# Performance work log

Measured on AMD Instinct MI355X. Metric: run time of the kernel, lower is better.

## Reference

```python
import jax, jax.numpy as jnp
import numpy as np

B, T, F = 32, 512, 4096
H = 128            # num_lstm
NUM_CLASSES = 2    # dense outputs = NUM_CLASSES + 1 (CTC blank)


def setup_inputs() -> dict:
    key = jax.random.key(0)
    ks = jax.random.split(key, 6)
    x = jax.random.normal(ks[0], (B, T, F), dtype=jnp.float32)
    # Keras LSTM params: kernel [F, 4H], recurrent_kernel [H, 4H], bias [4H]
    # (gate order i, f, c, o). Glorot-ish scaling for stability.
    Wk = jax.random.normal(ks[1], (F, 4 * H), dtype=jnp.float32) / np.sqrt(F)
    Wr = jax.random.normal(ks[2], (H, 4 * H), dtype=jnp.float32) / np.sqrt(H)
    b = jnp.zeros((4 * H,), dtype=jnp.float32).at[H:2 * H].set(1.0)  # unit_forget_bias
    Wd = jax.random.normal(ks[3], (H, NUM_CLASSES + 1), dtype=jnp.float32) / np.sqrt(H)
    bd = jnp.zeros((NUM_CLASSES + 1,), dtype=jnp.float32)
    return {"x": x, "Wk": Wk, "Wr": Wr, "b": b, "Wd": Wd, "bd": bd}


def _lstm(x, Wk, Wr, b):
    # Precompute input projections for all timesteps (big GEMM once).
    z = jnp.einsum("btf,fg->btg", x, Wk) + b          # [B, T, 4H]
    z = jnp.transpose(z, (1, 0, 2))                    # [T, B, 4H]

    def step(carry, z_t):
        h, c = carry
        g = z_t + h @ Wr                               # [B, 4H]
        i = jax.nn.sigmoid(g[:, 0 * H:1 * H])
        f = jax.nn.sigmoid(g[:, 1 * H:2 * H])
        cc = jnp.tanh(g[:, 2 * H:3 * H])
        o = jax.nn.sigmoid(g[:, 3 * H:4 * H])
        c = f * c + i * cc
        h = o * jnp.tanh(c)
        return (h, c), h

    h0 = jnp.zeros((x.shape[0], H), dtype=x.dtype)
    c0 = jnp.zeros((x.shape[0], H), dtype=x.dtype)
    _, hs = jax.lax.scan(step, (h0, c0), z)            # hs: [T, B, H]
    return jnp.transpose(hs, (1, 0, 2))                # [B, T, H]


def reference(x, Wk, Wr, b, Wd, bd):
    # Inference-mode forward (dropout/recurrent_dropout inactive).
    h = _lstm(x, Wk, Wr, b)                            # [B, T, H]
    return h @ Wd + bd                                 # [B, T, num_classes+1]
```

## Files before the change

### kernel.cpp

```cpp
#include <hip/hip_runtime.h>
#include <hip/hip_bf16.h>
#include <hip/hip_fp16.h>
#include <math.h>

#define B_  32
#define T_  512
#define F_  4096
#define H_  128
#define G4H 512
#define NCLS 3
#define M_  (B_ * T_)
#define KSTEPS 128

typedef _Float16 f16x8 __attribute__((ext_vector_type(8)));
typedef _Float16 f16x4 __attribute__((ext_vector_type(4)));
typedef float    f32x4 __attribute__((ext_vector_type(4)));

__global__ __launch_bounds__(256) void cvt_wkT(
    const float* __restrict__ Wk, _Float16* __restrict__ btK)
{
    __shared__ float ls[64][65];
    const int k0 = blockIdx.x * 64;
    const int n0 = blockIdx.y * 64;
    const int tid = threadIdx.x;

    {
        int r  = tid >> 4;
        int c4 = (tid & 15) * 4;
        #pragma unroll
        for (int p = 0; p < 4; ++p) {
            float4 v = *reinterpret_cast<const float4*>(
                &Wk[(size_t)(k0 + r + p * 16) * G4H + n0 + c4]);
            ls[r + p * 16][c4 + 0] = v.x;
            ls[r + p * 16][c4 + 1] = v.y;
            ls[r + p * 16][c4 + 2] = v.z;
            ls[r + p * 16][c4 + 3] = v.w;
        }
    }
    __syncthreads();
    {
        int rn = tid >> 2;
        int ck = (tid & 3) * 16;
        f16x8 h0, h1;
        #pragma unroll
        for (int j = 0; j < 8; ++j) {
            h0[j] = (_Float16)ls[ck + j][rn];
            h1[j] = (_Float16)ls[ck + 8 + j][rn];
        }
        const int n    = n0 + rn;
        const int kg   = k0 + ck;
        const int kblk = kg >> 5;
        const int kk   = kg & 31;
        const int g0   = kk >> 3;
        const int sw   = (n >> 1) & 3;
        _Float16* base = btK + (size_t)kblk * (512 * 32) + (size_t)n * 32;
        *reinterpret_cast<f16x8*>(base + ((g0 ^ sw) << 3))       = h0;
        *reinterpret_cast<f16x8*>(base + (((g0 + 1) ^ sw) << 3)) = h1;
    }
}

__global__ __launch_bounds__(256) void cvt_wrT(
    const float* __restrict__ Wr, _Float16* __restrict__ wrT)
{
    __shared__ float ls[64][65];
    const int k0 = blockIdx.x * 64;
    const int n0 = blockIdx.y * 64;
    const int tid = threadIdx.x;
    {
        int r  = tid >> 4;
        int c4 = (tid & 15) * 4;
        #pragma unroll
        for (int p = 0; p < 4; ++p) {
            float4 v = *reinterpret_cast<const float4*>(
                &Wr[(size_t)(k0 + r + p * 16) * G4H + n0 + c4]);
            ls[r + p * 16][c4 + 0] = v.x;
            ls[r + p * 16][c4 + 1] = v.y;
            ls[r + p * 16][c4 + 2] = v.z;
            ls[r + p * 16][c4 + 3] = v.w;
        }
    }
    __syncthreads();
    {
        int rn = tid >> 2;
        int ck = (tid & 3) * 16;
        f16x8 h0, h1;
        #pragma unroll
        for (int j = 0; j < 8; ++j) {
            h0[j] = (_Float16)ls[ck + j][rn];
            h1[j] = (_Float16)ls[ck + 8 + j][rn];
        }
        _Float16* dst = &wrT[(size_t)(n0 + rn) * H_ + k0 + ck];
        *reinterpret_cast<f16x8*>(dst)     = h0;
        *reinterpret_cast<f16x8*>(dst + 8) = h1;
    }
}

__device__ __forceinline__ void lds_barrier() {
    asm volatile("s_waitcnt lgkmcnt(0)" ::: "memory");
    __builtin_amdgcn_s_barrier();
    asm volatile("" ::: "memory");
}

__global__ __launch_bounds__(256, 4) void gemm_fused(
    const float* __restrict__ x, const _Float16* __restrict__ btK,
    const float* __restrict__ bias, float* __restrict__ z)
{
    __shared__ __align__(16) _Float16 As[2][64 * 32];

    const int tid = threadIdx.x;
    const int w   = tid >> 6;
    const int l   = tid & 63;
    const int fr  = l & 15;
    const int q   = l >> 4;

    const int bid   = blockIdx.x;
    const int xcd   = bid & 7;
    const int idx   = bid >> 3;
    const int mt    = xcd * 32 + (idx >> 2);
    const int ntile = idx & 3;
    const int m0    = mt * 64;
    const int n0    = ntile * 128;

    const int ar = tid >> 3;
    const int hc = (tid & 7) * 4;
    const int abyte = ((((hc >> 3) ^ ((ar >> 1) & 3)) << 4) | ((hc << 1) & 15));
    const float* xrow0 = x + (size_t)(m0 + ar) * F_ + hc;
    const float* xrow1 = xrow0 + (size_t)32 * F_;

    const int nA = n0 + w * 32 + fr;
    const int nB = nA + 16;
    const _Float16* bp0 = btK + (size_t)nA * 32 + ((q ^ ((nA >> 1) & 3)) << 3);
    const _Float16* bp1 = btK + (size_t)nB * 32 + ((q ^ ((nB >> 1) & 3)) << 3);

    #define LOADB(t, bfv)                                                     \
    {                                                                         \
        bfv[0] = *reinterpret_cast<const f16x8*>(bp0 + (size_t)(t) * 16384);  \
        bfv[1] = *reinterpret_cast<const f16x8*>(bp1 + (size_t)(t) * 16384);  \
    }

    #define LOADX(t, va, vb)                                                  \
    {                                                                         \
        va = *reinterpret_cast<const float4*>(xrow0 + (size_t)(t) * 32);      \
        vb = *reinterpret_cast<const float4*>(xrow1 + (size_t)(t) * 32);      \
    }

    #define WRITE_A(va, vb, buf)                                              \
    {                                                                         \
        f16x4 h0; h0[0] = (_Float16)va.x; h0[1] = (_Float16)va.y;             \
        h0[2] = (_Float16)va.z; h0[3] = (_Float16)va.w;                       \
        f16x4 h1; h1[0] = (_Float16)vb.x; h1[1] = (_Float16)vb.y;             \
        h1[2] = (_Float16)vb.z; h1[3] = (_Float16)vb.w;                       \
        char* ab = reinterpret_cast<char*>(&As[buf][0]);                      \
        *reinterpret_cast<f16x4*>(ab + ar * 64 + abyte) = h0;                 \
        *reinterpret_cast<f16x4*>(ab + (ar + 32) * 64 + abyte) = h1;          \
    }

    #define COMPUTE(buf, bfv)                                                 \
    {                                                                         \
        f16x8 af[4];                                                          \
        _Pragma("unroll")                                                     \
        for (int i = 0; i < 4; ++i) {                                         \
            int r   = i * 16 + fr;                                            \
            int off = r * 64 + ((q ^ ((r >> 1) & 3)) << 4);                   \
            af[i] = *reinterpret_cast<const f16x8*>(                          \
                reinterpret_cast<const char*>(&As[buf][0]) + off);            \
        }                                                                     \
        _Pragma("unroll")                                                     \
        for (int i = 0; i < 4; ++i)                                           \
            _Pragma("unroll")                                                 \
            for (int j = 0; j < 2; ++j)                                       \
                acc[i][j] = __builtin_amdgcn_mfma_f32_16x16x32_f16(           \
                    af[i], bfv[j], acc[i][j], 0, 0, 0);                       \
    }

    f32x4 acc[4][2] = {};
    f16x8 bfA[2], bfB[2];
    float4 xa0, xa1, xb0, xb1;

    LOADX(0, xa0, xa1) LOADX(1, xb0, xb1)
    LOADB(0, bfA) LOADB(1, bfB)
    WRITE_A(xa0, xa1, 0)
    lds_barrier();

    for (int t = 0; t < 126; t += 2) {
        LOADX(t + 2, xa0, xa1)
        WRITE_A(xb0, xb1, 1)
        COMPUTE(0, bfA)
        LOADB(t + 2, bfA)
        lds_barrier();
        LOADX(t + 3, xb0, xb1)
        WRITE_A(xa0, xa1, 0)
        COMPUTE(1, bfB)
        LOADB(t + 3, bfB)
        lds_barrier();
    }
    WRITE_A(xb0, xb1, 1)
    COMPUTE(0, bfA)
    lds_barrier();
    COMPUTE(1, bfB)

    #undef LOADB
    #undef LOADX
    #undef WRITE_A
    #undef COMPUTE

    #pragma unroll
    for (int j = 0; j < 2; ++j) {
        const int nn = n0 + w * 32 + j * 16 + fr;
        const float bj = bias[nn];
        #pragma unroll
        for (int i = 0; i < 4; ++i)
            #pragma unroll
            for (int r = 0; r < 4; ++r)
                z[(size_t)(m0 + i * 16 + q * 4 + r) * G4H + nn]
                    = acc[i][j][r] + bj;
    }
}

__device__ __forceinline__ float sig_f(float x) {
    return __builtin_amdgcn_rcpf(
        1.0f + __builtin_amdgcn_exp2f(-1.442695040888963f * x));
}
__device__ __forceinline__ float tanh_f(float x) {
    return 1.0f - 2.0f * __builtin_amdgcn_rcpf(
        1.0f + __builtin_amdgcn_exp2f(2.885390081777927f * x));
}

__global__ __launch_bounds__(512, 2) void lstm_mfma(
    const float* __restrict__ z,
    const _Float16* __restrict__ wrT,
    float* __restrict__ hs,
    float* __restrict__ cst,
    _Float16* __restrict__ h16,
    int t0)
{
    const int b    = blockIdx.x;
    const int tid  = threadIdx.x;
    const int w    = tid >> 6;
    const int lane = tid & 63;
    const int l15  = lane & 15;
    const int q    = lane >> 4;
    const int jj   = w * 16 + l15;

    __shared__ __align__(16) _Float16 hA[2][128];

    f16x8 bf[4][4];
    #pragma unroll
    for (int g = 0; g < 4; ++g)
        #pragma unroll
        for (int kf = 0; kf < 4; ++kf)
            bf[g][kf] = *reinterpret_cast<const f16x8*>(
                &wrT[(size_t)(g * H_ + jj) * H_ + kf * 32 + q * 8]);

    float cstate;
    if (t0 == 0) {
        if (tid < 128) reinterpret_cast<unsigned int*>(hA)[tid] = 0u;
        cstate = 0.f;
    } else {
        if (tid < 64)
            reinterpret_cast<unsigned int*>(hA[0])[tid] =
                reinterpret_cast<const unsigned int*>(h16 + (size_t)b * H_)[tid];
        cstate = cst[(size_t)b * H_ + jj];
    }

    const float* zq    = z  + (size_t)b * T_ * G4H + jj;
    float*       hbase = hs + (size_t)b * T_ * H_;

    const f32x4 zero4 = {0.f, 0.f, 0.f, 0.f};

    #define LOADZ(t, d)                                                       \
    {                                                                         \
        int zo = (((t) & (T_ - 1)) << 9);                                     \
        d.x = zq[zo];       d.y = zq[zo + 128];                               \
        d.z = zq[zo + 256]; d.w = zq[zo + 384];                               \
    }

    float4 zP0, zP1, zP2, zP3;
    LOADZ(t0 + 0, zP0) LOADZ(t0 + 1, zP1)
    LOADZ(t0 + 2, zP2) LOADZ(t0 + 3, zP3)

    __syncthreads();

    #define LSTM_STEP(t, CUR, ZZ)                                             \
    {                                                                         \
        f16x8 af0 = *reinterpret_cast<const f16x8*>(&hA[CUR][0 * 32 + q * 8]);\
        f16x8 af1 = *reinterpret_cast<const f16x8*>(&hA[CUR][1 * 32 + q * 8]);\
        f16x8 af2 = *reinterpret_cast<const f16x8*>(&hA[CUR][2 * 32 + q * 8]);\
        f16x8 af3 = *reinterpret_cast<const f16x8*>(&hA[CUR][3 * 32 + q * 8]);\
        float zt0_ = ZZ.x, zt1_ = ZZ.y, zt2_ = ZZ.z, zt3_ = ZZ.w;             \
        LOADZ((t) + 4, ZZ)                                                    \
        float gv[4];                                                          \
        _Pragma("unroll")                                                     \
        for (int g = 0; g < 4; ++g) {                                         \
            f32x4 aA = __builtin_amdgcn_mfma_f32_16x16x32_f16(                \
                af0, bf[g][0], zero4, 0, 0, 0);                               \
            aA = __builtin_amdgcn_mfma_f32_16x16x32_f16(                      \
                af1, bf[g][1], aA, 0, 0, 0);                                  \
            f32x4 aB = __builtin_amdgcn_mfma_f32_16x16x32_f16(                \
                af2, bf[g][2], zero4, 0, 0, 0);                               \
            aB = __builtin_amdgcn_mfma_f32_16x16x32_f16(                      \
                af3, bf[g][3], aB, 0, 0, 0);                                  \
            gv[g] = aA[0] + aB[0];                                            \
        }                                                                     \
        float iv = sig_f(gv[0] + zt0_);                                       \
        float fv = sig_f(gv[1] + zt1_);                                       \
        float cc = tanh_f(gv[2] + zt2_);                                      \
        float ov = sig_f(gv[3] + zt3_);                                       \
        cstate = fv * cstate + iv * cc;                                       \
        float h = ov * tanh_f(cstate);                                        \
        if (q == 0) {                                                         \
            hA[CUR ^ 1][jj] = (_Float16)h;                                    \
            hbase[((t) << 7) + jj] = h;                                       \
        }                                                                     \
        lds_barrier();                                                        \
    }

    for (int t = t0; t < t0 + 256; t += 4) {
        LSTM_STEP(t,     0, zP0)
        LSTM_STEP(t + 1, 1, zP1)
        LSTM_STEP(t + 2, 0, zP2)
        LSTM_STEP(t + 3, 1, zP3)
    }
    #undef LSTM_STEP
    #undef LOADZ

    if (q == 0) cst[(size_t)b * H_ + jj] = cstate;
    if (tid < 64)
        reinterpret_cast<unsigned int*>(h16 + (size_t)b * H_)[tid] =
            reinterpret_cast<unsigned int*>(hA[0])[tid];
}

__global__ __launch_bounds__(256) void dense_out(
    const float* __restrict__ hs, const float* __restrict__ Wd,
    const float* __restrict__ bd, float* __restrict__ out)
{
    int idx = blockIdx.x * 256 + threadIdx.x;
    if (idx >= B_ * T_ * NCLS) return;
    int cls = idx % NCLS;
    int row = idx / NCLS;
    const float* h = hs + (size_t)row * H_;
    float acc = bd[cls];
    #pragma unroll 8
    for (int k = 0; k < H_; ++k) acc += h[k] * Wd[k * NCLS + cls];
    out[idx] = acc;
}

extern "C" void kernel_launch(void* const* d_in, const int* in_sizes, int n_in,
                              void* d_out, int out_size, void* d_ws, size_t ws_size,
                              hipStream_t stream)
{
    const float* x  = (const float*)d_in[0];
    const float* Wk = (const float*)d_in[1];
    const float* Wr = (const float*)d_in[2];
    const float* b  = (const float*)d_in[3];
    const float* Wd = (const float*)d_in[4];
    const float* bd = (const float*)d_in[5];
    float* out = (float*)d_out;

    float*     z   = (float*)d_ws;
    float*     hs  = z + (size_t)M_ * G4H;
    _Float16*  btK = (_Float16*)(hs + (size_t)M_ * H_);
    _Float16*  wrT = btK + (size_t)G4H * F_;
    float*     cst = (float*)(wrT + (size_t)G4H * H_);
    _Float16*  h16 = (_Float16*)(cst + (size_t)B_ * H_);

    cvt_wkT<<<dim3(F_ / 64, G4H / 64), 256, 0, stream>>>(Wk, btK);
    cvt_wrT<<<dim3(H_ / 64, G4H / 64), 256, 0, stream>>>(Wr, wrT);
    gemm_fused<<<1024, 256, 0, stream>>>(x, btK, b, z);
    lstm_mfma<<<B_, 512, 0, stream>>>(z, wrT, hs, cst, h16, 0);
    lstm_mfma<<<B_, 512, 0, stream>>>(z, wrT, hs, cst, h16, 256);
    int total = B_ * T_ * NCLS;
    dense_out<<<(total + 255) / 256, 256, 0, stream>>>(hs, Wd, bd, out);
}
```

Baseline: 434.2 us.

## Widen input-projection GEMM tile to 256 columns and batch four k-steps per barrier

The input-projection GEMM now uses 512-thread blocks that each compute a 64x256 output tile, so every x tile is converted to fp16 for two column tiles instead of four. This halves redundant global reads of the large fp32 input. The LDS buffer now holds four k-slices per stage, so one barrier covers four MFMA k-steps instead of one. The cost is more LDS per block, and __launch_bounds__(512, 4) may cap registers tightly enough to cause spills or lower occupancy.

```diff
diff --git a/kernel.cpp b/kernel.cpp
--- a/kernel.cpp
+++ b/kernel.cpp
@@ -101,11 +101,11 @@
     asm volatile("" ::: "memory");
 }
 
-__global__ __launch_bounds__(256, 4) void gemm_fused(
+__global__ __launch_bounds__(512, 4) void gemm_fused(
     const float* __restrict__ x, const _Float16* __restrict__ btK,
     const float* __restrict__ bias, float* __restrict__ z)
 {
-    __shared__ __align__(16) _Float16 As[2][64 * 32];
+    __shared__ __align__(16) _Float16 As[2][4][64 * 32];
 
     const int tid = threadIdx.x;
     const int w   = tid >> 6;
@@ -116,16 +116,15 @@
     const int bid   = blockIdx.x;
     const int xcd   = bid & 7;
     const int idx   = bid >> 3;
-    const int mt    = xcd * 32 + (idx >> 2);
-    const int ntile = idx & 3;
+    const int mt    = xcd * 32 + (idx >> 1);
+    const int ntile = idx & 1;
     const int m0    = mt * 64;
-    const int n0    = ntile * 128;
+    const int n0    = ntile * 256;
 
     const int ar = tid >> 3;
     const int hc = (tid & 7) * 4;
     const int abyte = ((((hc >> 3) ^ ((ar >> 1) & 3)) << 4) | ((hc << 1) & 15));
-    const float* xrow0 = x + (size_t)(m0 + ar) * F_ + hc;
-    const float* xrow1 = xrow0 + (size_t)32 * F_;
+    const float* xrow = x + (size_t)(m0 + ar) * F_ + hc;
 
     const int nA = n0 + w * 32 + fr;
     const int nB = nA + 16;
@@ -138,24 +137,17 @@
         bfv[1] = *reinterpret_cast<const f16x8*>(bp1 + (size_t)(t) * 16384);  \
     }
 
-    #define LOADX(t, va, vb)                                                  \
-    {                                                                         \
-        va = *reinterpret_cast<const float4*>(xrow0 + (size_t)(t) * 32);      \
-        vb = *reinterpret_cast<const float4*>(xrow1 + (size_t)(t) * 32);      \
-    }
-
-    #define WRITE_A(va, vb, buf)                                              \
-    {                                                                         \
-        f16x4 h0; h0[0] = (_Float16)va.x; h0[1] = (_Float16)va.y;             \
-        h0[2] = (_Float16)va.z; h0[3] = (_Float16)va.w;                       \
-        f16x4 h1; h1[0] = (_Float16)vb.x; h1[1] = (_Float16)vb.y;             \
-        h1[2] = (_Float16)vb.z; h1[3] = (_Float16)vb.w;                       \
-        char* ab = reinterpret_cast<char*>(&As[buf][0]);                      \
-        *reinterpret_cast<f16x4*>(ab + ar * 64 + abyte) = h0;                 \
-        *reinterpret_cast<f16x4*>(ab + (ar + 32) * 64 + abyte) = h1;          \
-    }
-
-    #define COMPUTE(buf, bfv)                                                 \
+    #define LOADX(t) (*reinterpret_cast<const float4*>(xrow + (size_t)(t) * 32))
+
+    #define WRITE_A(v, G, s)                                                  \
+    {                                                                         \
+        f16x4 hh; hh[0] = (_Float16)v.x; hh[1] = (_Float16)v.y;               \
+        hh[2] = (_Float16)v.z; hh[3] = (_Float16)v.w;                         \
+        *reinterpret_cast<f16x4*>(                                            \
+            reinterpret_cast<char*>(&As[G][s][0]) + ar * 64 + abyte) = hh;    \
+    }
+
+    #define COMPUTE(G, s, bfv)                                                \
     {                                                                         \
         f16x8 af[4];                                                          \
         _Pragma("unroll")                                                     \
@@ -163,7 +155,7 @@
             int r   = i * 16 + fr;                                            \
             int off = r * 64 + ((q ^ ((r >> 1) & 3)) << 4);                   \
             af[i] = *reinterpret_cast<const f16x8*>(                          \
-                reinterpret_cast<const char*>(&As[buf][0]) + off);            \
+                reinterpret_cast<const char*>(&As[G][s][0]) + off);           \
         }                                                                     \
         _Pragma("unroll")                                                     \
         for (int i = 0; i < 4; ++i)                                           \
@@ -173,36 +165,54 @@
                     af[i], bfv[j], acc[i][j], 0, 0, 0);                       \
     }
 
+    #define GROUP(t0, G)                                                      \
+    {                                                                         \
+        WRITE_A(xq0, G ^ 1, 0) WRITE_A(xq1, G ^ 1, 1)                         \
+        WRITE_A(xq2, G ^ 1, 2) WRITE_A(xq3, G ^ 1, 3)                         \
+        xq0 = LOADX((t0) + 8);  xq1 = LOADX((t0) + 9);                        \
+        xq2 = LOADX((t0) + 10); xq3 = LOADX((t0) + 11);                       \
+        COMPUTE(G, 0, bfA) LOADB((t0) + 2, bfA)                               \
+        COMPUTE(G, 1, bfB) LOADB((t0) + 3, bfB)                               \
+        COMPUTE(G, 2, bfA) LOADB((t0) + 4, bfA)                               \
+        COMPUTE(G, 3, bfB) LOADB((t0) + 5, bfB)                               \
+        lds_barrier();                                                        \
+    }
+
     f32x4 acc[4][2] = {};
     f16x8 bfA[2], bfB[2];
-    float4 xa0, xa1, xb0, xb1;
-
-    LOADX(0, xa0, xa1) LOADX(1, xb0, xb1)
+    float4 xq0, xq1, xq2, xq3;
+
+    xq0 = LOADX(0); xq1 = LOADX(1); xq2 = LOADX(2); xq3 = LOADX(3);
+    WRITE_A(xq0, 0, 0) WRITE_A(xq1, 0, 1) WRITE_A(xq2, 0, 2) WRITE_A(xq3, 0, 3)
+    xq0 = LOADX(4); xq1 = LOADX(5); xq2 = LOADX(6); xq3 = LOADX(7);
     LOADB(0, bfA) LOADB(1, bfB)
-    WRITE_A(xa0, xa1, 0)
     lds_barrier();
 
-    for (int t = 0; t < 126; t += 2) {
-        LOADX(t + 2, xa0, xa1)
-        WRITE_A(xb0, xb1, 1)
-        COMPUTE(0, bfA)
-        LOADB(t + 2, bfA)
+    for (int gg = 0; gg < 30; gg += 2) {
+        const int t0 = gg * 4;
+        GROUP(t0, 0)
+        GROUP(t0 + 4, 1)
+    }
+    {
+        WRITE_A(xq0, 1, 0) WRITE_A(xq1, 1, 1) WRITE_A(xq2, 1, 2) WRITE_A(xq3, 1, 3)
+        COMPUTE(0, 0, bfA) LOADB(122, bfA)
+        COMPUTE(0, 1, bfB) LOADB(123, bfB)
+        COMPUTE(0, 2, bfA) LOADB(124, bfA)
+        COMPUTE(0, 3, bfB) LOADB(125, bfB)
         lds_barrier();
-        LOADX(t + 3, xb0, xb1)
-        WRITE_A(xa0, xa1, 0)
-        COMPUTE(1, bfB)
-        LOADB(t + 3, bfB)
-        lds_barrier();
-    }
-    WRITE_A(xb0, xb1, 1)
-    COMPUTE(0, bfA)
-    lds_barrier();
-    COMPUTE(1, bfB)
+    }
+    {
+        COMPUTE(1, 0, bfA) LOADB(126, bfA)
+        COMPUTE(1, 1, bfB) LOADB(127, bfB)
+        COMPUTE(1, 2, bfA)
+        COMPUTE(1, 3, bfB)
+    }
 
     #undef LOADB
     #undef LOADX
     #undef WRITE_A
     #undef COMPUTE
+    #undef GROUP
 
     #pragma unroll
     for (int j = 0; j < 2; ++j) {
@@ -366,7 +376,7 @@
 
     cvt_wkT<<<dim3(F_ / 64, G4H / 64), 256, 0, stream>>>(Wk, btK);
     cvt_wrT<<<dim3(H_ / 64, G4H / 64), 256, 0, stream>>>(Wr, wrT);
-    gemm_fused<<<1024, 256, 0, stream>>>(x, btK, b, z);
+    gemm_fused<<<512, 512, 0, stream>>>(x, btK, b, z);
     lstm_mfma<<<B_, 512, 0, stream>>>(z, wrT, hs, cst, h16, 0);
     lstm_mfma<<<B_, 512, 0, stream>>>(z, wrT, hs, cst, h16, 256);
     int total = B_ * T_ * NCLS;
```

After: 357.5 us. 1.21x faster.
